# Kernel optimization log

Measured on AMD Instinct MI355X. Metric: run time of the kernel, lower is better.

The kernel has to match this reference:

```python
import jax, jax.numpy as jnp
import numpy as np


def setup_inputs() -> dict:
    key = jax.random.key(0)
    # [N, n, m]: batch, transform length (axis 1), columns
    x = jax.random.normal(key, (32, 1024, 512), dtype=jnp.float32)
    return {"x": x}


def reference(x):
    # Faithful port of idct_odd_case: IDCT-III via a length-2n complex IFFT
    # on a Hermitian-symmetric-style mirrored array, exactly as the TF code.
    N, n, m = x.shape
    k = jnp.arange(n, dtype=jnp.float32)
    # t[k] = sqrt(2n) * exp(i*pi*k/(2n)); t[0] scaled by extra sqrt(2)
    t = jnp.sqrt(2.0 * n) * jnp.exp(1j * k * (np.pi / (2.0 * n)))
    t = t.at[0].multiply(jnp.sqrt(2.0))
    W = t.astype(jnp.complex64)[None, :, None]           # [1, n, 1]
    xc = x.astype(jnp.complex64)
    yy_up = W * xc                                        # [N, n, m]
    # -i * W[1:n] * reverse(x[1:n]) along the transform axis
    yy_down = (-1j) * W[:, 1:, :] * xc[:, n - 1:0:-1, :]  # [N, n-1, m]
    yy_mid = jnp.zeros((N, 1, m), dtype=jnp.complex64)
    yy = jnp.concatenate([yy_up, yy_mid, yy_down], axis=1)  # [N, 2n, m]
    y = jnp.fft.ifft(yy, axis=1)                          # matlab_ifft: ifft on axis 1
    return jnp.real(y[:, :n, :]).astype(jnp.float32)
```

## Files before the change

### kernel.cpp

```cpp
#include <hip/hip_runtime.h>

typedef unsigned short u16;
typedef __attribute__((ext_vector_type(8))) __bf16 bf16x8;
typedef __attribute__((ext_vector_type(4))) float f32x4;

#define GLOAD_LDS16(g, l)                                                                     \
  __builtin_amdgcn_global_load_lds((const __attribute__((address_space(1))) unsigned int*)(g), \
                                   (__attribute__((address_space(3))) unsigned int*)(l), 16, 0, 0)

static __device__ __forceinline__ u16 f2bf(float f) {
  unsigned int u = __float_as_uint(f);
  u += 0x7fffu + ((u >> 16) & 1u);
  return (u16)(u >> 16);
}

#define BATCH 32
#define NN 1024
#define MM 512

static __device__ __forceinline__ int swz(int r) { return ((r >> 1) ^ ((r & 1) << 2)) & 7; }

__global__ void fill_g(u16* __restrict__ G) {
  int idx = blockIdx.x * 256 + threadIdx.x;
  int jt  = idx >> 17;
  int s   = (idx >> 13) & 15;
  int row = (idx >> 6) & 127;
  int pc  = (idx >> 3) & 7;
  int sub = idx & 7;
  int dc = pc ^ (row & 7);
  int j = jt * 128 + row;
  int k;
  if (dc < 4) k = 2 * (s * 32 + dc * 8 + sub);
  else        k = 2 * (s * 32 + (dc - 4) * 8 + sub) + 1;
  float v;
  if (k == 0) {
    v = 0.03125f;
  } else {
    int ph = (k * (2 * j + 1)) & 4095;
    v = 0.04419417382415922f * cosf((float)ph * 1.5339807878856412e-3f);
  }
  G[idx] = f2bf(v);
}

__global__ __launch_bounds__(256, 2) void gemm_idct(const u16* __restrict__ G,
                                                    const float* __restrict__ X,
                                                    float* __restrict__ C) {
  __shared__ __align__(16) u16 sA[2][8192];
  __shared__ __align__(16) u16 sX[4096];
  const int wg    = blockIdx.x;
  const int xcd   = wg & 7;
  const int local = wg >> 3;
  const int jt    = local & 3;
  const int pg    = xcd * 32 + (local >> 2);
  const int ct    = pg & 7;
  const int b     = pg >> 3;

  const int t = threadIdx.x;
  const int wave = t >> 6, lane = t & 63;
  const int wm = wave >> 1, wn = wave & 1;
  const int lhi = lane >> 4, llo = lane & 15;

  const u16* gA = G + (size_t)jt * 131072 + t * 8;
#define ISSUE_A(buf, s)                                                        \
  do {                                                                         \
    _Pragma("unroll") for (int cl = 0; cl < 4; ++cl)                           \
      GLOAD_LDS16(gA + (s) * 8192 + cl * 2048, &sA[buf][cl * 2048 + t * 8]);   \
  } while (0)

  const int c2 = (t & 31) << 1;
  const int kq = t >> 5;
  const float* gX = X + ((size_t)b * NN + kq * 8) * MM + ct * 64 + c2;

#define LOAD_X(s, XR)                                                          \
  do {                                                                         \
    const float* p = gX + (size_t)(s) * 64 * MM;                               \
    _Pragma("unroll") for (int i = 0; i < 8; ++i)                              \
      XR[i] = *(const float2*)(p + (size_t)i * MM);                            \
  } while (0)

#define WRITE_X(XR)                                                            \
  do {                                                                         \
    _Pragma("unroll") for (int cc = 0; cc < 2; ++cc) {                         \
      const int row = c2 + cc;                                                 \
      const int f = swz(row);                                                  \
      ushort4 e, o;                                                            \
      e.x = f2bf(cc ? XR[0].y : XR[0].x); o.x = f2bf(cc ? XR[1].y : XR[1].x);  \
      e.y = f2bf(cc ? XR[2].y : XR[2].x); o.y = f2bf(cc ? XR[3].y : XR[3].x);  \
      e.z = f2bf(cc ? XR[4].y : XR[4].x); o.z = f2bf(cc ? XR[5].y : XR[5].x);  \
      e.w = f2bf(cc ? XR[6].y : XR[6].x); o.w = f2bf(cc ? XR[7].y : XR[7].x);  \
      const int slot = (kq & 1) << 2;                                          \
      *(ushort4*)&sX[row * 64 + (((kq >> 1) ^ f) << 3) + slot] = e;            \
      *(ushort4*)&sX[row * 64 + (((4 + (kq >> 1)) ^ f) << 3) + slot] = o;      \
    }                                                                          \
  } while (0)

  f32x4 accE[4][2] = {};
  f32x4 accO[4][2] = {};
  float2 xrA[8], xrB[8];

#define STEP(s, XR)                                                            \
  do {                                                                         \
    WRITE_X(XR);          \
    if ((s) < 15)                                                              \
      asm volatile("s_waitcnt vmcnt(8) lgkmcnt(0)" ::: "memory");              \
    else                                                                       \
      asm volatile("s_waitcnt vmcnt(0) lgkmcnt(0)" ::: "memory");              \
    __builtin_amdgcn_sched_barrier(0);                                         \
    __builtin_amdgcn_s_barrier();         \
    __builtin_amdgcn_sched_barrier(0);                                         \
    if ((s) < 15) ISSUE_A(((s) + 1) & 1, (s) + 1);                             \
    if ((s) < 14) LOAD_X((s) + 2, XR);                                         \
    {                                                                          \
      const u16* lA = &sA[(s) & 1][0];                                         \
      bf16x8 fe[4], fo[4], fxe[2], fxo[2];                                     \
      _Pragma("unroll") for (int mf = 0; mf < 4; ++mf) {                       \
        const int ra = wm * 64 + mf * 16 + llo;                                \
        const int fa = ra & 7;                                                 \
        fe[mf] = *(const bf16x8*)&lA[ra * 64 + ((lhi ^ fa) << 3)];             \
        fo[mf] = *(const bf16x8*)&lA[ra * 64 + (((4 + lhi) ^ fa) << 3)];       \
      }                                                                        \
      _Pragma("unroll") for (int nf = 0; nf < 2; ++nf) {                       \
        const int rb = wn * 32 + nf * 16 + llo;                                \
        const int fb = swz(rb);                                                \
        fxe[nf] = *(const bf16x8*)&sX[rb * 64 + ((lhi ^ fb) << 3)];            \
        fxo[nf] = *(const bf16x8*)&sX[rb * 64 + (((4 + lhi) ^ fb) << 3)];      \
      }                                                                        \
      __builtin_amdgcn_s_setprio(1);                                           \
      _Pragma("unroll") for (int mf = 0; mf < 4; ++mf)                         \
        _Pragma("unroll") for (int nf = 0; nf < 2; ++nf)                       \
          accE[mf][nf] = __builtin_amdgcn_mfma_f32_16x16x32_bf16(              \
              fe[mf], fxe[nf], accE[mf][nf], 0, 0, 0);                         \
      _Pragma("unroll") for (int mf = 0; mf < 4; ++mf)                         \
        _Pragma("unroll") for (int nf = 0; nf < 2; ++nf)                       \
          accO[mf][nf] = __builtin_amdgcn_mfma_f32_16x16x32_bf16(              \
              fo[mf], fxo[nf], accO[mf][nf], 0, 0, 0);                         \
      __builtin_amdgcn_s_setprio(0);                                           \
    }                                                                          \
    __builtin_amdgcn_sched_barrier(0);                                         \
    __builtin_amdgcn_s_barrier();                                \
    __builtin_amdgcn_sched_barrier(0);                                         \
  } while (0)

  LOAD_X(0, xrA);
  ISSUE_A(0, 0);
  LOAD_X(1, xrB);

#pragma unroll
  for (int ss = 0; ss < 8; ++ss) {
    STEP(2 * ss,     xrA);
    STEP(2 * ss + 1, xrB);
  }

  float* Cb = C + (size_t)b * NN * MM;
  const int cbase = ct * 64 + wn * 32 + llo;
#pragma unroll
  for (int mf = 0; mf < 4; ++mf)
#pragma unroll
    for (int nf = 0; nf < 2; ++nf) {
      const int jh0 = jt * 128 + wm * 64 + mf * 16 + lhi * 4;
      const int c   = cbase + nf * 16;
#pragma unroll
      for (int r = 0; r < 4; ++r) {
        const float ye = accE[mf][nf][r];
        const float yo = accO[mf][nf][r];
        const int j = jh0 + r;
        Cb[(size_t)j * MM + c]            = ye + yo;
        Cb[(size_t)(NN - 1 - j) * MM + c] = ye - yo;
      }
    }
#undef ISSUE_A
#undef LOAD_X
#undef WRITE_X
#undef STEP
}

extern "C" void kernel_launch(void* const* d_in, const int* in_sizes, int n_in,
                              void* d_out, int out_size, void* d_ws, size_t ws_size,
                              hipStream_t stream) {
  const float* x = (const float*)d_in[0];
  float* out = (float*)d_out;
  u16* G = (u16*)d_ws;

  fill_g<<<dim3(2048), dim3(256), 0, stream>>>(G);
  gemm_idct<<<dim3(1024), dim3(256), 0, stream>>>(G, x, out);
}
```

Measured before the change: 49.04 us.

## Halve GEMM row tile to 64, triple-buffer A, raise occupancy to 4

The output row tile per workgroup drops from 128 to 64, so the grid doubles to 2048 blocks, each accumulating a 2x2 fragment grid per wave. The G matrix layout and fill kernel are re-indexed to match. A prefetching moves from double to triple buffering, two stages ahead, and launch bounds allow 4 blocks per CU. X loads change to scalar float loads with 16 rows per thread and a single 16-byte LDS write. The goal is more parallelism and latency hiding, at the cost of loading and converting X twice as often overall and having less MFMA work per LDS load.

```diff
diff --git a/kernel.cpp b/kernel.cpp
--- a/kernel.cpp
+++ b/kernel.cpp
@@ -22,13 +22,13 @@
 
 __global__ void fill_g(u16* __restrict__ G) {
   int idx = blockIdx.x * 256 + threadIdx.x;
-  int jt  = idx >> 17;
-  int s   = (idx >> 13) & 15;
-  int row = (idx >> 6) & 127;
+  int jt  = idx >> 16;
+  int s   = (idx >> 12) & 15;
+  int row = (idx >> 6) & 63;
   int pc  = (idx >> 3) & 7;
   int sub = idx & 7;
   int dc = pc ^ (row & 7);
-  int j = jt * 128 + row;
+  int j = jt * 64 + row;
   int k;
   if (dc < 4) k = 2 * (s * 32 + dc * 8 + sub);
   else        k = 2 * (s * 32 + (dc - 4) * 8 + sub) + 1;
@@ -42,16 +42,16 @@
   G[idx] = f2bf(v);
 }
 
-__global__ __launch_bounds__(256, 2) void gemm_idct(const u16* __restrict__ G,
+__global__ __launch_bounds__(256, 4) void gemm_idct(const u16* __restrict__ G,
                                                     const float* __restrict__ X,
                                                     float* __restrict__ C) {
-  __shared__ __align__(16) u16 sA[2][8192];
+  __shared__ __align__(16) u16 sA[3][4096];
   __shared__ __align__(16) u16 sX[4096];
   const int wg    = blockIdx.x;
   const int xcd   = wg & 7;
   const int local = wg >> 3;
-  const int jt    = local & 3;
-  const int pg    = xcd * 32 + (local >> 2);
+  const int jt    = local & 7;
+  const int pg    = xcd * 32 + (local >> 3);
   const int ct    = pg & 7;
   const int b     = pg >> 3;
 
@@ -60,61 +60,59 @@
   const int wm = wave >> 1, wn = wave & 1;
   const int lhi = lane >> 4, llo = lane & 15;
 
-  const u16* gA = G + (size_t)jt * 131072 + t * 8;
+  const u16* gA = G + (size_t)jt * 65536 + t * 8;
 #define ISSUE_A(buf, s)                                                        \
   do {                                                                         \
-    _Pragma("unroll") for (int cl = 0; cl < 4; ++cl)                           \
-      GLOAD_LDS16(gA + (s) * 8192 + cl * 2048, &sA[buf][cl * 2048 + t * 8]);   \
+    GLOAD_LDS16(gA + (s) * 4096,        &sA[buf][t * 8]);                      \
+    GLOAD_LDS16(gA + (s) * 4096 + 2048, &sA[buf][2048 + t * 8]);               \
   } while (0)
 
-  const int c2 = (t & 31) << 1;
-  const int kq = t >> 5;
-  const float* gX = X + ((size_t)b * NN + kq * 8) * MM + ct * 64 + c2;
+  const int cx = t & 63;
+  const int kq = t >> 6;
+  const float* gX = X + ((size_t)b * NN + kq * 16) * MM + ct * 64 + cx;
 
 #define LOAD_X(s, XR)                                                          \
   do {                                                                         \
     const float* p = gX + (size_t)(s) * 64 * MM;                               \
-    _Pragma("unroll") for (int i = 0; i < 8; ++i)                              \
-      XR[i] = *(const float2*)(p + (size_t)i * MM);                            \
+    _Pragma("unroll") for (int i = 0; i < 16; ++i)                             \
+      XR[i] = p[(size_t)i * MM];                                               \
   } while (0)
 
 #define WRITE_X(XR)                                                            \
   do {                                                                         \
-    _Pragma("unroll") for (int cc = 0; cc < 2; ++cc) {                         \
-      const int row = c2 + cc;                                                 \
-      const int f = swz(row);                                                  \
-      ushort4 e, o;                                                            \
-      e.x = f2bf(cc ? XR[0].y : XR[0].x); o.x = f2bf(cc ? XR[1].y : XR[1].x);  \
-      e.y = f2bf(cc ? XR[2].y : XR[2].x); o.y = f2bf(cc ? XR[3].y : XR[3].x);  \
-      e.z = f2bf(cc ? XR[4].y : XR[4].x); o.z = f2bf(cc ? XR[5].y : XR[5].x);  \
-      e.w = f2bf(cc ? XR[6].y : XR[6].x); o.w = f2bf(cc ? XR[7].y : XR[7].x);  \
-      const int slot = (kq & 1) << 2;                                          \
-      *(ushort4*)&sX[row * 64 + (((kq >> 1) ^ f) << 3) + slot] = e;            \
-      *(ushort4*)&sX[row * 64 + (((4 + (kq >> 1)) ^ f) << 3) + slot] = o;      \
+    const int f = swz(cx);                                                     \
+    bf16x8 e, o;                                                               \
+    _Pragma("unroll") for (int m = 0; m < 8; ++m) {                            \
+      e[m] = (__bf16)XR[2 * m];                                                \
+      o[m] = (__bf16)XR[2 * m + 1];                                            \
     }                                                                          \
+    *(bf16x8*)&sX[cx * 64 + ((kq ^ f) << 3)] = e;                              \
+    *(bf16x8*)&sX[cx * 64 + (((4 + kq) ^ f) << 3)] = o;                        \
   } while (0)
 
-  f32x4 accE[4][2] = {};
-  f32x4 accO[4][2] = {};
-  float2 xrA[8], xrB[8];
+  f32x4 accE[2][2] = {};
+  f32x4 accO[2][2] = {};
+  float xrA[16], xrB[16];
 
 #define STEP(s, XR)                                                            \
   do {                                                                         \
-    WRITE_X(XR);          \
+    WRITE_X(XR);                                \
     if ((s) < 15)                                                              \
-      asm volatile("s_waitcnt vmcnt(8) lgkmcnt(0)" ::: "memory");              \
+      asm volatile("s_waitcnt vmcnt(18) lgkmcnt(0)" ::: "memory");             \
     else                                                                       \
       asm volatile("s_waitcnt vmcnt(0) lgkmcnt(0)" ::: "memory");              \
     __builtin_amdgcn_sched_barrier(0);                                         \
-    __builtin_amdgcn_s_barrier();         \
+    __builtin_amdgcn_s_barrier();       \
     __builtin_amdgcn_sched_barrier(0);                                         \
-    if ((s) < 15) ISSUE_A(((s) + 1) & 1, (s) + 1);                             \
-    if ((s) < 14) LOAD_X((s) + 2, XR);                                         \
+    if ((s) < 14) {                                                            \
+      ISSUE_A((s + 2) % 3, (s) + 2);                                           \
+      LOAD_X((s) + 2, XR);                                                     \
+    }                                                                          \
     {                                                                          \
-      const u16* lA = &sA[(s) & 1][0];                                         \
-      bf16x8 fe[4], fo[4], fxe[2], fxo[2];                                     \
-      _Pragma("unroll") for (int mf = 0; mf < 4; ++mf) {                       \
-        const int ra = wm * 64 + mf * 16 + llo;                                \
+      const u16* lA = &sA[(s) % 3][0];                                         \
+      bf16x8 fe[2], fo[2], fxe[2], fxo[2];                                     \
+      _Pragma("unroll") for (int mf = 0; mf < 2; ++mf) {                       \
+        const int ra = wm * 32 + mf * 16 + llo;                                \
         const int fa = ra & 7;                                                 \
         fe[mf] = *(const bf16x8*)&lA[ra * 64 + ((lhi ^ fa) << 3)];             \
         fo[mf] = *(const bf16x8*)&lA[ra * 64 + (((4 + lhi) ^ fa) << 3)];       \
@@ -126,24 +124,25 @@
         fxo[nf] = *(const bf16x8*)&sX[rb * 64 + (((4 + lhi) ^ fb) << 3)];      \
       }                                                                        \
       __builtin_amdgcn_s_setprio(1);                                           \
-      _Pragma("unroll") for (int mf = 0; mf < 4; ++mf)                         \
+      _Pragma("unroll") for (int mf = 0; mf < 2; ++mf)                         \
         _Pragma("unroll") for (int nf = 0; nf < 2; ++nf)                       \
           accE[mf][nf] = __builtin_amdgcn_mfma_f32_16x16x32_bf16(              \
               fe[mf], fxe[nf], accE[mf][nf], 0, 0, 0);                         \
-      _Pragma("unroll") for (int mf = 0; mf < 4; ++mf)                         \
+      _Pragma("unroll") for (int mf = 0; mf < 2; ++mf)                         \
         _Pragma("unroll") for (int nf = 0; nf < 2; ++nf)                       \
           accO[mf][nf] = __builtin_amdgcn_mfma_f32_16x16x32_bf16(              \
               fo[mf], fxo[nf], accO[mf][nf], 0, 0, 0);                         \
       __builtin_amdgcn_s_setprio(0);                                           \
     }                                                                          \
     __builtin_amdgcn_sched_barrier(0);                                         \
-    __builtin_amdgcn_s_barrier();                                \
+    __builtin_amdgcn_s_barrier();  \
     __builtin_amdgcn_sched_barrier(0);                                         \
   } while (0)
 
   LOAD_X(0, xrA);
   ISSUE_A(0, 0);
   LOAD_X(1, xrB);
+  ISSUE_A(1, 1);
 
 #pragma unroll
   for (int ss = 0; ss < 8; ++ss) {
@@ -154,10 +153,10 @@
   float* Cb = C + (size_t)b * NN * MM;
   const int cbase = ct * 64 + wn * 32 + llo;
 #pragma unroll
-  for (int mf = 0; mf < 4; ++mf)
+  for (int mf = 0; mf < 2; ++mf)
 #pragma unroll
     for (int nf = 0; nf < 2; ++nf) {
-      const int jh0 = jt * 128 + wm * 64 + mf * 16 + lhi * 4;
+      const int jh0 = jt * 64 + wm * 32 + mf * 16 + lhi * 4;
       const int c   = cbase + nf * 16;
 #pragma unroll
       for (int r = 0; r < 4; ++r) {
@@ -182,5 +181,5 @@
   u16* G = (u16*)d_ws;
 
   fill_g<<<dim3(2048), dim3(256), 0, stream>>>(G);
-  gemm_idct<<<dim3(1024), dim3(256), 0, stream>>>(G, x, out);
+  gemm_idct<<<dim3(2048), dim3(256), 0, stream>>>(G, x, out);
 }
```

Result: slower. 50.40 us (+2.8%).

## Double K-step depth to 128 and restructure X staging with per-column loads

Applied to the files above, without the earlier changes.

Each pipeline stage now covers a K chunk of 128 instead of 64, so there are 8 stages instead of 16. The LDS buffers for G and X are doubled and the G fill layout is rewritten to match, with even and odd halves per row. X is now loaded as 32 scalar floats per thread along the transform axis, in place of float2 pairs, and written to LDS as bf16x8 vectors. The aim is to halve the number of barriers and stages per tile. In exchange the kernel uses more LDS and registers, drops the two-stage X register prefetch, and waits on vmcnt implicitly, which may expose global load latency.

```diff
diff --git a/kernel.cpp b/kernel.cpp
--- a/kernel.cpp
+++ b/kernel.cpp
@@ -22,16 +22,17 @@
 
 __global__ void fill_g(u16* __restrict__ G) {
   int idx = blockIdx.x * 256 + threadIdx.x;
-  int jt  = idx >> 17;
-  int s   = (idx >> 13) & 15;
-  int row = (idx >> 6) & 127;
-  int pc  = (idx >> 3) & 7;
-  int sub = idx & 7;
+  int jt   = idx >> 17;
+  int s    = (idx >> 14) & 7;
+  int row  = (idx >> 7) & 127;
+  int rest = idx & 127;
+  int eo   = rest >> 6;
+  int pc   = (rest >> 3) & 7;
+  int sub  = rest & 7;
   int dc = pc ^ (row & 7);
+  int p = s * 64 + dc * 8 + sub;
+  int k = 2 * p + eo;
   int j = jt * 128 + row;
-  int k;
-  if (dc < 4) k = 2 * (s * 32 + dc * 8 + sub);
-  else        k = 2 * (s * 32 + (dc - 4) * 8 + sub) + 1;
   float v;
   if (k == 0) {
     v = 0.03125f;
@@ -45,8 +46,8 @@
 __global__ __launch_bounds__(256, 2) void gemm_idct(const u16* __restrict__ G,
                                                     const float* __restrict__ X,
                                                     float* __restrict__ C) {
-  __shared__ __align__(16) u16 sA[2][8192];
-  __shared__ __align__(16) u16 sX[4096];
+  __shared__ __align__(16) u16 sA[2][16384];
+  __shared__ __align__(16) u16 sX[8192];
   const int wg    = blockIdx.x;
   const int xcd   = wg & 7;
   const int local = wg >> 3;
@@ -63,93 +64,89 @@
   const u16* gA = G + (size_t)jt * 131072 + t * 8;
 #define ISSUE_A(buf, s)                                                        \
   do {                                                                         \
-    _Pragma("unroll") for (int cl = 0; cl < 4; ++cl)                           \
-      GLOAD_LDS16(gA + (s) * 8192 + cl * 2048, &sA[buf][cl * 2048 + t * 8]);   \
+    _Pragma("unroll") for (int cl = 0; cl < 8; ++cl)                           \
+      GLOAD_LDS16(gA + (s) * 16384 + cl * 2048, &sA[buf][cl * 2048 + t * 8]);  \
   } while (0)
 
-  const int c2 = (t & 31) << 1;
-  const int kq = t >> 5;
-  const float* gX = X + ((size_t)b * NN + kq * 8) * MM + ct * 64 + c2;
+  const int cx = t & 63;
+  const int kq = t >> 6;
+  const float* gX = X + ((size_t)b * NN + kq * 32) * MM + ct * 64 + cx;
 
-#define LOAD_X(s, XR)                                                          \
+  float xr[32];
+#define LOAD_X(s)                                                              \
   do {                                                                         \
-    const float* p = gX + (size_t)(s) * 64 * MM;                               \
-    _Pragma("unroll") for (int i = 0; i < 8; ++i)                              \
-      XR[i] = *(const float2*)(p + (size_t)i * MM);                            \
+    const float* p = gX + (size_t)(s) * 128 * MM;                              \
+    _Pragma("unroll") for (int i = 0; i < 32; ++i)                             \
+      xr[i] = p[(size_t)i * MM];                                               \
   } while (0)
 
-#define WRITE_X(XR)                                                            \
+#define WRITE_X()                                                              \
   do {                                                                         \
-    _Pragma("unroll") for (int cc = 0; cc < 2; ++cc) {                         \
-      const int row = c2 + cc;                                                 \
-      const int f = swz(row);                                                  \
-      ushort4 e, o;                                                            \
-      e.x = f2bf(cc ? XR[0].y : XR[0].x); o.x = f2bf(cc ? XR[1].y : XR[1].x);  \
-      e.y = f2bf(cc ? XR[2].y : XR[2].x); o.y = f2bf(cc ? XR[3].y : XR[3].x);  \
-      e.z = f2bf(cc ? XR[4].y : XR[4].x); o.z = f2bf(cc ? XR[5].y : XR[5].x);  \
-      e.w = f2bf(cc ? XR[6].y : XR[6].x); o.w = f2bf(cc ? XR[7].y : XR[7].x);  \
-      const int slot = (kq & 1) << 2;                                          \
-      *(ushort4*)&sX[row * 64 + (((kq >> 1) ^ f) << 3) + slot] = e;            \
-      *(ushort4*)&sX[row * 64 + (((4 + (kq >> 1)) ^ f) << 3) + slot] = o;      \
+    const int f = swz(cx);                                                     \
+    _Pragma("unroll") for (int h = 0; h < 2; ++h) {                            \
+      bf16x8 e, o;                                                             \
+      _Pragma("unroll") for (int i = 0; i < 8; ++i) {                          \
+        e[i] = (__bf16)xr[16 * h + 2 * i];                                     \
+        o[i] = (__bf16)xr[16 * h + 2 * i + 1];                                 \
+      }                                                                        \
+      const int ch = (2 * kq + h) ^ f;                                         \
+      *(bf16x8*)&sX[cx * 128 + ch * 8] = e;                                    \
+      *(bf16x8*)&sX[cx * 128 + 64 + ch * 8] = o;                               \
     }                                                                          \
   } while (0)
 
   f32x4 accE[4][2] = {};
   f32x4 accO[4][2] = {};
-  float2 xrA[8], xrB[8];
 
-#define STEP(s, XR)                                                            \
+#define STEP(s)                                                                \
   do {                                                                         \
-    WRITE_X(XR);          \
-    if ((s) < 15)                                                              \
-      asm volatile("s_waitcnt vmcnt(8) lgkmcnt(0)" ::: "memory");              \
-    else                                                                       \
-      asm volatile("s_waitcnt vmcnt(0) lgkmcnt(0)" ::: "memory");              \
+    WRITE_X();                       \
+    asm volatile("s_waitcnt lgkmcnt(0)" ::: "memory");                         \
     __builtin_amdgcn_sched_barrier(0);                                         \
-    __builtin_amdgcn_s_barrier();         \
+    __builtin_amdgcn_s_barrier();       \
     __builtin_amdgcn_sched_barrier(0);                                         \
-    if ((s) < 15) ISSUE_A(((s) + 1) & 1, (s) + 1);                             \
-    if ((s) < 14) LOAD_X((s) + 2, XR);                                         \
+    if ((s) < 7) {                                                             \
+      ISSUE_A(((s) + 1) & 1, (s) + 1);                                         \
+      LOAD_X((s) + 1);                                                         \
+    }                                                                          \
     {                                                                          \
       const u16* lA = &sA[(s) & 1][0];                                         \
-      bf16x8 fe[4], fo[4], fxe[2], fxo[2];                                     \
-      _Pragma("unroll") for (int mf = 0; mf < 4; ++mf) {                       \
-        const int ra = wm * 64 + mf * 16 + llo;                                \
-        const int fa = ra & 7;                                                 \
-        fe[mf] = *(const bf16x8*)&lA[ra * 64 + ((lhi ^ fa) << 3)];             \
-        fo[mf] = *(const bf16x8*)&lA[ra * 64 + (((4 + lhi) ^ fa) << 3)];       \
+      _Pragma("unroll") for (int ks = 0; ks < 2; ++ks) {                       \
+        bf16x8 fe[4], fo[4], fxe[2], fxo[2];                                   \
+        _Pragma("unroll") for (int mf = 0; mf < 4; ++mf) {                     \
+          const int ra = wm * 64 + mf * 16 + llo;                              \
+          const int ca = ((ks * 4 + lhi) ^ (ra & 7)) << 3;                     \
+          fe[mf] = *(const bf16x8*)&lA[ra * 128 + ca];                         \
+          fo[mf] = *(const bf16x8*)&lA[ra * 128 + 64 + ca];                    \
+        }                                                                      \
+        _Pragma("unroll") for (int nf = 0; nf < 2; ++nf) {                     \
+          const int rb = wn * 32 + nf * 16 + llo;                              \
+          const int cb = ((ks * 4 + lhi) ^ swz(rb)) << 3;                      \
+          fxe[nf] = *(const bf16x8*)&sX[rb * 128 + cb];                        \
+          fxo[nf] = *(const bf16x8*)&sX[rb * 128 + 64 + cb];                   \
+        }                                                                      \
+        __builtin_amdgcn_s_setprio(1);                                         \
+        _Pragma("unroll") for (int mf = 0; mf < 4; ++mf)                       \
+          _Pragma("unroll") for (int nf = 0; nf < 2; ++nf)                     \
+            accE[mf][nf] = __builtin_amdgcn_mfma_f32_16x16x32_bf16(            \
+                fe[mf], fxe[nf], accE[mf][nf], 0, 0, 0);                       \
+        _Pragma("unroll") for (int mf = 0; mf < 4; ++mf)                       \
+          _Pragma("unroll") for (int nf = 0; nf < 2; ++nf)                     \
+            accO[mf][nf] = __builtin_amdgcn_mfma_f32_16x16x32_bf16(            \
+                fo[mf], fxo[nf], accO[mf][nf], 0, 0, 0);                       \
+        __builtin_amdgcn_s_setprio(0);                                         \
       }                                                                        \
-      _Pragma("unroll") for (int nf = 0; nf < 2; ++nf) {                       \
-        const int rb = wn * 32 + nf * 16 + llo;                                \
-        const int fb = swz(rb);                                                \
-        fxe[nf] = *(const bf16x8*)&sX[rb * 64 + ((lhi ^ fb) << 3)];            \
-        fxo[nf] = *(const bf16x8*)&sX[rb * 64 + (((4 + lhi) ^ fb) << 3)];      \
-      }                                                                        \
-      __builtin_amdgcn_s_setprio(1);                                           \
-      _Pragma("unroll") for (int mf = 0; mf < 4; ++mf)                         \
-        _Pragma("unroll") for (int nf = 0; nf < 2; ++nf)                       \
-          accE[mf][nf] = __builtin_amdgcn_mfma_f32_16x16x32_bf16(              \
-              fe[mf], fxe[nf], accE[mf][nf], 0, 0, 0);                         \
-      _Pragma("unroll") for (int mf = 0; mf < 4; ++mf)                         \
-        _Pragma("unroll") for (int nf = 0; nf < 2; ++nf)                       \
-          accO[mf][nf] = __builtin_amdgcn_mfma_f32_16x16x32_bf16(              \
-              fo[mf], fxo[nf], accO[mf][nf], 0, 0, 0);                         \
-      __builtin_amdgcn_s_setprio(0);                                           \
     }                                                                          \
     __builtin_amdgcn_sched_barrier(0);                                         \
-    __builtin_amdgcn_s_barrier();                                \
+    __builtin_amdgcn_s_barrier();       \
     __builtin_amdgcn_sched_barrier(0);                                         \
   } while (0)
 
-  LOAD_X(0, xrA);
   ISSUE_A(0, 0);
-  LOAD_X(1, xrB);
+  LOAD_X(0);
 
-#pragma unroll
-  for (int ss = 0; ss < 8; ++ss) {
-    STEP(2 * ss,     xrA);
-    STEP(2 * ss + 1, xrB);
-  }
+  STEP(0); STEP(1); STEP(2); STEP(3);
+  STEP(4); STEP(5); STEP(6); STEP(7);
 
   float* Cb = C + (size_t)b * NN * MM;
   const int cbase = ct * 64 + wn * 32 + llo;
```

After: 44.78 us, median of 2. 1.1x faster.
